# Performance work log

Hardware: AMD Instinct MI355X
Metric: run time of the kernel (lower is better)

The kernel has to match this reference:

```python
import jax, jax.numpy as jnp
import numpy as np

N_PATCH, N_Z, K, BS = 16, 128, 10, 1024
D = N_PATCH * N_Z


def setup_inputs() -> dict:
    key = jax.random.key(0)
    k1, k2, k3, k4 = jax.random.split(key, 4)
    z = jax.random.normal(k1, (BS, D), dtype=jnp.float32)
    m = jax.random.normal(k2, (K, D), dtype=jnp.float32)
    L = jax.random.normal(k3, (K, D, D), dtype=jnp.float32)
    components = jax.random.randint(k4, (BS,), 0, K, dtype=jnp.int64)
    return {"z": z, "m": m, "L": L, "components": components}


def reference(z, m, L, components):
    # samps[k] = m[k] + z @ L[k].T   -> (K, BS, D)
    samps = jnp.einsum('bd,ked->kbe', z, L) + m[:, None, :]
    # one-hot mask-and-sum over components == gather selected expert per sample
    x = samps[components, jnp.arange(z.shape[0])]  # (BS, D)
    return x.reshape(-1, N_PATCH, N_Z)
```

## Files before the change

### kernel.cpp

```cpp
#include <hip/hip_runtime.h>
#include <hip/hip_bf16.h>


#define DDIM  2048
#define BSAMP 1024
#define KCOMP 10
#define MPAD  160
#define NT    32
#define BK    32
#define NITER (DDIM / BK)
#define TILEP 12288
#define BBYTES 4096
#define NBUF  3
#define NXCD  8
#define NWG   (KCOMP * (DDIM / NT))

typedef __attribute__((ext_vector_type(8))) short bf16x8;
typedef __attribute__((ext_vector_type(4))) float f32x4;

__device__ __forceinline__ void async16(void* lds, const void* g) {
    __builtin_amdgcn_global_load_lds(
        (const __attribute__((address_space(1))) void*)g,
        (__attribute__((address_space(3))) void*)lds, 16, 0, 0);
}

__device__ __forceinline__ short bfs(float x) {
    __hip_bfloat16 h = __float2bfloat16(x);
    return *reinterpret_cast<short*>(&h);
}

__device__ __forceinline__ bf16x8 gld16(const void* p) {
    bf16x8 r;
    asm volatile("global_load_dwordx4 %0, %1, off" : "=v"(r) : "v"(p));
    return r;
}

__global__ void build_map(const int* __restrict__ comp,
                          int* __restrict__ rowmap,
                          int* __restrict__ counts) {
    __shared__ int sc[KCOMP];
    const int t = threadIdx.x;
    if (t < KCOMP) sc[t] = 0;
    __syncthreads();
    const int c = comp[t];
    const int r = atomicAdd(&sc[c], 1);
    if (r < MPAD) rowmap[c * MPAD + r] = t;
    __syncthreads();
    if (t < KCOMP) counts[t] = sc[t];
}

__global__ void zgather(const float* __restrict__ z,
                        const int* __restrict__ rowmap,
                        short* __restrict__ zb) {
    const int k  = blockIdx.x;
    const int sp = blockIdx.y;
    const int t  = threadIdx.x;
    const int c  = t & 7;
    const int g  = c & 3;
    const int s0 = rowmap[k * MPAD + 2 * sp]     & (BSAMP - 1);
    const int s1 = rowmap[k * MPAD + 2 * sp + 1] & (BSAMP - 1);
    const int src = (c >> 2) ? s1 : s0;
    const int swz = (c ^ (sp & 7)) * 16;
    char* kbase = (char*)zb + (size_t)k * NITER * TILEP + sp * 128 + swz;
#pragma unroll
    for (int p = 0; p < 2; ++p) {
        const int it = p * 32 + (t >> 3);
        const float* zr = z + (size_t)src * DDIM + it * BK + g * 8;
        f32x4 x = *(const f32x4*)zr;
        f32x4 y = *(const f32x4*)(zr + 4);
        bf16x8 r;
#pragma unroll
        for (int i = 0; i < 4; ++i) { r[i] = bfs(x[i]); r[4 + i] = bfs(y[i]); }
        *(bf16x8*)(kbase + (size_t)it * TILEP) = r;
    }
}

__global__ __launch_bounds__(256, 4)
void gmm_gemm(const short* __restrict__ zb,
              const float* __restrict__ mvec,
              const float* __restrict__ Lmat,
              const int* __restrict__ rowmap,
              const int* __restrict__ counts,
              float* __restrict__ out) {
    __shared__ __attribute__((aligned(16))) char smem[NBUF * BBYTES];
    const int t    = threadIdx.x;
    const int lane = t & 63;
    const int w    = t >> 6;
    const int mh   = w >> 1;
    const int nh   = w & 1;
    const int lin  = blockIdx.x;
    const int newlin = (lin & (NXCD - 1)) * (NWG / NXCD) + (lin >> 3);
    const int k    = newlin >> 6;
    const int n0   = (newlin & 63) * NT;
    const float* Lk = Lmat + (size_t)k * DDIM * DDIM;
    const char* zt  = (const char*)zb + (size_t)k * NITER * TILEP;
    const int cnt  = counts[k];

    int mtmax = (cnt - mh * 80 + 15) >> 4;
    mtmax = mtmax < 0 ? 0 : (mtmax > 5 ? 5 : mtmax);

    const int br = t >> 3,          bc = ((t & 7) ^ (br & 7)) * 4;
    const unsigned ub = (unsigned)(t & ~63) * 16;

    const int fr = lane & 15;
    const int g  = lane >> 4;
    const int rb = nh * 16 + fr;
    const int h0 = ((2 * g)     ^ (rb & 7)) * 4;
    const int h1 = ((2 * g + 1) ^ (rb & 7)) * 4;
    const int frh = fr >> 1;
    const int fra = (fr & 1) * 4 + g;
    const char* za = zt + mh * 5120 + frh * 128 + ((fra ^ frh) * 16);

    f32x4 acc[5];
#pragma unroll
    for (int mt = 0; mt < 5; ++mt) acc[mt] = (f32x4){0.f, 0.f, 0.f, 0.f};

    bf16x8 a0[5], a1[5];

    auto stageB = [&](int bi, int it) {
        async16(smem + bi * BBYTES + ub,
                Lk + (size_t)(n0 + br) * DDIM + it * BK + bc);
    };
    auto loadA = [&](bf16x8 (&a)[5], int it) {
        const char* p = za + (size_t)it * TILEP;
#pragma unroll
        for (int mt = 0; mt < 5; ++mt) a[mt] = gld16(p + mt * 1024);
    };
    auto computeB = [&](int bi) {
        const float* B = (const float*)(smem + bi * BBYTES);
        f32x4 x = *(const f32x4*)(B + rb * 32 + h0);
        f32x4 y = *(const f32x4*)(B + rb * 32 + h1);
        bf16x8 bb;
#pragma unroll
        for (int i = 0; i < 4; ++i) { bb[i] = bfs(x[i]); bb[4 + i] = bfs(y[i]); }
        return bb;
    };
    auto mfma5 = [&](bf16x8 (&a)[5], bf16x8 bb) {
#pragma unroll
        for (int mt = 0; mt < 5; ++mt)
            if (mt < mtmax)
                acc[mt] = __builtin_amdgcn_mfma_f32_16x16x32_bf16(a[mt], bb, acc[mt], 0, 0, 0);
    };

    stageB(0, 0); loadA(a0, 0); stageB(1, 1); loadA(a1, 1); stageB(2, 2);

    int bi = 0;
    for (int j = 0; j < 60; j += 2) {
        asm volatile("s_waitcnt vmcnt(12)" ::: "memory");
        __builtin_amdgcn_s_barrier();
        {
            bf16x8 bb = computeB(bi);
            asm volatile("s_waitcnt vmcnt(6)" ::: "memory");
            __builtin_amdgcn_sched_barrier(0);
            mfma5(a0, bb);
        }
        loadA(a0, j + 2);
        __builtin_amdgcn_s_barrier();
        stageB(bi, j + 3);
        bi = (bi == NBUF - 1) ? 0 : bi + 1;
        asm volatile("s_waitcnt vmcnt(12)" ::: "memory");
        __builtin_amdgcn_s_barrier();
        {
            bf16x8 bb = computeB(bi);
            asm volatile("s_waitcnt vmcnt(6)" ::: "memory");
            __builtin_amdgcn_sched_barrier(0);
            mfma5(a1, bb);
        }
        loadA(a1, j + 3);
        __builtin_amdgcn_s_barrier();
        stageB(bi, j + 4);
        bi = (bi == NBUF - 1) ? 0 : bi + 1;
    }
    asm volatile("s_waitcnt vmcnt(12)" ::: "memory");
    __builtin_amdgcn_s_barrier();
    {
        bf16x8 bb = computeB(bi);
        asm volatile("s_waitcnt vmcnt(6)" ::: "memory");
        __builtin_amdgcn_sched_barrier(0);
        mfma5(a0, bb);
    }
    loadA(a0, 62);
    __builtin_amdgcn_s_barrier();
    stageB(bi, 63);
    bi = (bi == NBUF - 1) ? 0 : bi + 1;
    asm volatile("s_waitcnt vmcnt(12)" ::: "memory");
    __builtin_amdgcn_s_barrier();
    {
        bf16x8 bb = computeB(bi);
        asm volatile("s_waitcnt vmcnt(6)" ::: "memory");
        __builtin_amdgcn_sched_barrier(0);
        mfma5(a1, bb);
    }
    loadA(a1, 63);
    __builtin_amdgcn_s_barrier();
    bi = (bi == NBUF - 1) ? 0 : bi + 1;
    asm volatile("s_waitcnt vmcnt(11)" ::: "memory");
    __builtin_amdgcn_s_barrier();
    {
        bf16x8 bb = computeB(bi);
        asm volatile("s_waitcnt vmcnt(6)" ::: "memory");
        __builtin_amdgcn_sched_barrier(0);
        mfma5(a0, bb);
    }
    __builtin_amdgcn_s_barrier();
    bi = (bi == NBUF - 1) ? 0 : bi + 1;
    asm volatile("s_waitcnt vmcnt(5)" ::: "memory");
    __builtin_amdgcn_s_barrier();
    {
        bf16x8 bb = computeB(bi);
        asm volatile("s_waitcnt vmcnt(0)" ::: "memory");
        __builtin_amdgcn_sched_barrier(0);
        mfma5(a1, bb);
    }

    const int rquad = g * 4;
    const int e  = n0 + nh * 16 + fr;
    const float mu = mvec[k * DDIM + e];
#pragma unroll
    for (int mt = 0; mt < 5; ++mt) {
        if (mt < mtmax) {
            const int sb = mh * 80 + mt * 16 + rquad;
#pragma unroll
            for (int r = 0; r < 4; ++r) {
                const int slot = sb + r;
                if (slot < cnt) {
                    const int b = rowmap[k * MPAD + slot];
                    out[(size_t)b * DDIM + e] = acc[mt][r] + mu;
                }
            }
        }
    }
}

extern "C" void kernel_launch(void* const* d_in, const int* in_sizes, int n_in,
                              void* d_out, int out_size, void* d_ws, size_t ws_size,
                              hipStream_t stream) {
    const float* z    = (const float*)d_in[0];
    const float* mvec = (const float*)d_in[1];
    const float* Lmat = (const float*)d_in[2];
    const int* comp   = (const int*)d_in[3];
    float* out        = (float*)d_out;

    int* rowmap = (int*)d_ws;
    int* counts = rowmap + KCOMP * MPAD;
    short* zb   = (short*)((char*)d_ws + 8192);

    build_map<<<1, BSAMP, 0, stream>>>(comp, rowmap, counts);
    zgather<<<dim3(KCOMP, MPAD / 2), 256, 0, stream>>>(z, rowmap, zb);
    gmm_gemm<<<NWG, 256, 0, stream>>>(zb, mvec, Lmat, rowmap, counts, out);
}
```

Measured before the change: 273.1 us.

## Split GEMM reduction dimension four ways with last-arriver partial-sum reduction

Splits the K-dimension loop of the per-component GEMM into four chunks, launching four times as many workgroups. Each writes its fp32 partial tile to a workspace buffer, bumps an atomic counter per output tile, and the last arriving workgroup sums the partials, adds the mean, and scatters to the output. This targets low occupancy or tail effects from the original 640-workgroup grid. The cost is extra partial-sum traffic to global memory, atomics, and more pipeline prologue/epilogue overhead per block.

Result: slower. 823.9 us (+201.7%).

```diff
diff --git a/kernel.cpp b/kernel.cpp
--- a/kernel.cpp
+++ b/kernel.cpp
@@ -9,11 +9,14 @@
 #define NT    32
 #define BK    32
 #define NITER (DDIM / BK)
+#define SPLITS 4
+#define NS    (NITER / SPLITS)
 #define TILEP 12288
 #define BBYTES 4096
 #define NBUF  3
 #define NXCD  8
-#define NWG   (KCOMP * (DDIM / NT))
+#define NWG   (KCOMP * 64 * SPLITS)
+#define PSZ   (MPAD * NT)
 
 typedef __attribute__((ext_vector_type(8))) short bf16x8;
 typedef __attribute__((ext_vector_type(4))) float f32x4;
@@ -37,10 +40,12 @@
 
 __global__ void build_map(const int* __restrict__ comp,
                           int* __restrict__ rowmap,
-                          int* __restrict__ counts) {
+                          int* __restrict__ counts,
+                          int* __restrict__ flags) {
     __shared__ int sc[KCOMP];
     const int t = threadIdx.x;
     if (t < KCOMP) sc[t] = 0;
+    if (t < KCOMP * 64) flags[t] = 0;
     __syncthreads();
     const int c = comp[t];
     const int r = atomicAdd(&sc[c], 1);
@@ -81,8 +86,11 @@
               const float* __restrict__ Lmat,
               const int* __restrict__ rowmap,
               const int* __restrict__ counts,
-              float* __restrict__ out) {
+              float* __restrict__ out,
+              float* __restrict__ partials,
+              int* __restrict__ flags) {
     __shared__ __attribute__((aligned(16))) char smem[NBUF * BBYTES];
+    __shared__ int s_old;
     const int t    = threadIdx.x;
     const int lane = t & 63;
     const int w    = t >> 6;
@@ -90,8 +98,12 @@
     const int nh   = w & 1;
     const int lin  = blockIdx.x;
     const int newlin = (lin & (NXCD - 1)) * (NWG / NXCD) + (lin >> 3);
-    const int k    = newlin >> 6;
-    const int n0   = (newlin & 63) * NT;
+    const int s    = newlin & 3;
+    const int nt   = (newlin >> 2) & 63;
+    const int k    = newlin >> 8;
+    const int n0   = nt * NT;
+    const int tb   = s * NS;
+    const int group = newlin >> 2;
     const float* Lk = Lmat + (size_t)k * DDIM * DDIM;
     const char* zt  = (const char*)zb + (size_t)k * NITER * TILEP;
     const int cnt  = counts[k];
@@ -119,10 +131,10 @@
 
     auto stageB = [&](int bi, int it) {
         async16(smem + bi * BBYTES + ub,
-                Lk + (size_t)(n0 + br) * DDIM + it * BK + bc);
+                Lk + (size_t)(n0 + br) * DDIM + (tb + it) * BK + bc);
     };
     auto loadA = [&](bf16x8 (&a)[5], int it) {
-        const char* p = za + (size_t)it * TILEP;
+        const char* p = za + (size_t)(tb + it) * TILEP;
 #pragma unroll
         for (int mt = 0; mt < 5; ++mt) a[mt] = gld16(p + mt * 1024);
     };
@@ -145,7 +157,7 @@
     stageB(0, 0); loadA(a0, 0); stageB(1, 1); loadA(a1, 1); stageB(2, 2);
 
     int bi = 0;
-    for (int j = 0; j < 60; j += 2) {
+    for (int j = 0; j < NS - 4; j += 2) {
         asm volatile("s_waitcnt vmcnt(12)" ::: "memory");
         __builtin_amdgcn_s_barrier();
         {
@@ -158,6 +170,7 @@
         __builtin_amdgcn_s_barrier();
         stageB(bi, j + 3);
         bi = (bi == NBUF - 1) ? 0 : bi + 1;
+
         asm volatile("s_waitcnt vmcnt(12)" ::: "memory");
         __builtin_amdgcn_s_barrier();
         {
@@ -179,9 +192,9 @@
         __builtin_amdgcn_sched_barrier(0);
         mfma5(a0, bb);
     }
-    loadA(a0, 62);
-    __builtin_amdgcn_s_barrier();
-    stageB(bi, 63);
+    loadA(a0, NS - 2);
+    __builtin_amdgcn_s_barrier();
+    stageB(bi, NS - 1);
     bi = (bi == NBUF - 1) ? 0 : bi + 1;
     asm volatile("s_waitcnt vmcnt(12)" ::: "memory");
     __builtin_amdgcn_s_barrier();
@@ -191,7 +204,7 @@
         __builtin_amdgcn_sched_barrier(0);
         mfma5(a1, bb);
     }
-    loadA(a1, 63);
+    loadA(a1, NS - 1);
     __builtin_amdgcn_s_barrier();
     bi = (bi == NBUF - 1) ? 0 : bi + 1;
     asm volatile("s_waitcnt vmcnt(11)" ::: "memory");
@@ -214,18 +227,44 @@
     }
 
     const int rquad = g * 4;
-    const int e  = n0 + nh * 16 + fr;
-    const float mu = mvec[k * DDIM + e];
+    const int lcol  = nh * 16 + fr;
+    const int e     = n0 + lcol;
+    float* Pg = partials + (size_t)group * (SPLITS * PSZ);
+    float* Ps = Pg + s * PSZ;
 #pragma unroll
     for (int mt = 0; mt < 5; ++mt) {
         if (mt < mtmax) {
             const int sb = mh * 80 + mt * 16 + rquad;
 #pragma unroll
-            for (int r = 0; r < 4; ++r) {
-                const int slot = sb + r;
-                if (slot < cnt) {
-                    const int b = rowmap[k * MPAD + slot];
-                    out[(size_t)b * DDIM + e] = acc[mt][r] + mu;
+            for (int r = 0; r < 4; ++r)
+                Ps[(sb + r) * NT + lcol] = acc[mt][r];
+        }
+    }
+    __threadfence();
+    if (t == 0)
+        s_old = __hip_atomic_fetch_add(&flags[group], 1, __ATOMIC_ACQ_REL,
+                                       __HIP_MEMORY_SCOPE_AGENT);
+    __syncthreads();
+    if (s_old == SPLITS - 1) {
+        const float mu = mvec[k * DDIM + e];
+#pragma unroll
+        for (int mt = 0; mt < 5; ++mt) {
+            if (mt < mtmax) {
+                const int sb = mh * 80 + mt * 16 + rquad;
+#pragma unroll
+                for (int r = 0; r < 4; ++r) {
+                    const int slot = sb + r;
+                    if (slot < cnt) {
+                        float sum = acc[mt][r];
+#pragma unroll
+                        for (int q = 1; q < SPLITS; ++q) {
+                            float* pp = Pg + ((s + q) & 3) * PSZ + slot * NT + lcol;
+                            sum += __hip_atomic_load(pp, __ATOMIC_RELAXED,
+                                                     __HIP_MEMORY_SCOPE_AGENT);
+                        }
+                        const int b = rowmap[k * MPAD + slot];
+                        out[(size_t)b * DDIM + e] = sum + mu;
+                    }
                 }
             }
         }
@@ -243,9 +282,16 @@
 
     int* rowmap = (int*)d_ws;
     int* counts = rowmap + KCOMP * MPAD;
-    short* zb   = (short*)((char*)d_ws + 8192);
-
-    build_map<<<1, BSAMP, 0, stream>>>(comp, rowmap, counts);
+    const size_t zb_off = 8192;
+    const size_t zb_bytes = (size_t)KCOMP * NITER * TILEP;
+    const size_t pt_off = zb_off + zb_bytes;
+    const size_t pt_bytes = (size_t)KCOMP * 64 * SPLITS * PSZ * 4;
+    short* zb       = (short*)((char*)d_ws + zb_off);
+    float* partials = (float*)((char*)d_ws + pt_off);
+    int*   flags    = (int*)((char*)d_ws + pt_off + pt_bytes);
+
+    build_map<<<1, BSAMP, 0, stream>>>(comp, rowmap, counts, flags);
     zgather<<<dim3(KCOMP, MPAD / 2), 256, 0, stream>>>(z, rowmap, zb);
-    gmm_gemm<<<NWG, 256, 0, stream>>>(zb, mvec, Lmat, rowmap, counts, out);
-}
+    gmm_gemm<<<NWG, 256, 0, stream>>>(zb, mvec, Lmat, rowmap, counts, out,
+                                      partials, flags);
+}
```
